# Optimization experiments

Hardware: AMD Instinct MI355X
Metric: run time of the kernel (lower is better)

Reference implementation:

```python
import jax, jax.numpy as jnp
import numpy as np

WINDOW_LEN = 512
N_VAR = 64
LOW_RANK = 16
BATCH = 512


def setup_inputs() -> dict:
    key = jax.random.key(0)
    k_x, k_g, k_b, k_A, k_B = jax.random.split(key, 5)
    x = jax.random.normal(k_x, (BATCH, WINDOW_LEN, N_VAR, 1), dtype=jnp.float32)
    # gating initialized at gating_init in the module; use small positive values
    gating = 0.01 * jnp.ones((N_VAR,), dtype=jnp.float32)
    # bias initialized to zeros in the module, but give it random values so the
    # residual path is exercised numerically
    bias = 0.02 * jax.random.normal(k_b, (WINDOW_LEN, N_VAR), dtype=jnp.float32)
    # kaiming-uniform-ish scale for lora_A: bound = sqrt(6 / fan_in) / sqrt(1+a^2) with a=sqrt(5)
    bound = np.sqrt(6.0 / LOW_RANK) / np.sqrt(6.0)
    lora_A = jax.random.uniform(k_A, (WINDOW_LEN, LOW_RANK), dtype=jnp.float32,
                                minval=-bound, maxval=bound)
    # lora_B is zero-init in the module; use small random values for a nontrivial test
    lora_B = 0.02 * jax.random.normal(k_B, (LOW_RANK, WINDOW_LEN, N_VAR), dtype=jnp.float32)
    return {"x": x, "gating": gating, "bias": bias, "lora_A": lora_A, "lora_B": lora_B}


def reference(x, gating, bias, lora_A, lora_B):
    # x: [b, t, n, d] with t == window_len and n*d == n_var (var_wise=True path)
    b, t, n, d = x.shape
    xr = x.reshape(b, t, n * d)                     # [b, t, v]
    x1 = jnp.tanh(gating * xr)                      # gate per variable, [b, t, v]
    # Original computes weight = einsum('ik,kjl->ijl', lora_A, lora_B)  (dense [t,t,v])
    # then einsum('biv,iov->bov', x1, weight). Same math via associativity:
    tmp = jnp.einsum('biv,ik->bkv', x1, lora_A)     # [b, r, v]
    new_x = jnp.einsum('bkv,kov->bov', tmp, lora_B) # [b, t, v]
    out = xr + new_x + bias                          # residual + bias
    return out.reshape(b, t, n, d)
```

## Files before the change

kernel.cpp:

```cpp
#include <hip/hip_runtime.h>

#define WL 512
#define NV 64
#define LR 16
#define NB 512

__device__ __forceinline__ float tanh_fast(float x) {
    float e = __expf(2.0f * x);
    return 1.0f - 2.0f / (e + 1.0f);
}

__global__ __launch_bounds__(512, 2) void k_tmp(
    const float* __restrict__ x, const float* __restrict__ gating,
    const float* __restrict__ A, float* __restrict__ tmp)
{
    __shared__ float A_lds[WL * LR];
    __shared__ float red[8 * LR * NV];
    const int tid = threadIdx.x;
    const int b = blockIdx.x;

    {
        const float4* src = (const float4*)(A + tid * LR);
        float4* dst = (float4*)(A_lds + tid * LR);
        dst[0] = src[0]; dst[1] = src[1]; dst[2] = src[2]; dst[3] = src[3];
    }
    __syncthreads();

    const int v = tid & 63;
    const int tg = tid >> 6;
    const float g = gating[v];
    float acc[LR];
#pragma unroll
    for (int k = 0; k < LR; ++k) acc[k] = 0.f;

    const float* xb = x + (size_t)b * WL * NV;
    for (int i = 0; i < 64; ++i) {
        const int t = tg * 64 + i;
        const float x1 = tanh_fast(g * xb[t * NV + v]);
        const float* Ar = &A_lds[t * LR];
#pragma unroll
        for (int k = 0; k < LR; ++k) acc[k] += x1 * Ar[k];
    }

#pragma unroll
    for (int k = 0; k < LR; ++k) red[(tg * LR + k) * NV + v] = acc[k];
    __syncthreads();
#pragma unroll
    for (int p = tid; p < LR * NV; p += 512) {
        float s = 0.f;
#pragma unroll
        for (int t = 0; t < 8; ++t) s += red[t * (LR * NV) + p];
        tmp[(size_t)b * (LR * NV) + p] = s;
    }
}

__global__ __launch_bounds__(256, 4) void k_out(
    const float* __restrict__ x, const float* __restrict__ bias,
    const float* __restrict__ Bm, const float* __restrict__ tmp,
    float* __restrict__ out)
{
    const int tid = threadIdx.x;
    const int v = tid & 63;
    const int og = tid >> 6;
    const int o_base = blockIdx.y * 16 + og * 4;
    const int b0 = blockIdx.x * 8;

    float Breg[4][LR];
#pragma unroll
    for (int j = 0; j < 4; ++j) {
        const int o = o_base + j;
#pragma unroll
        for (int k = 0; k < LR; ++k)
            Breg[j][k] = Bm[((size_t)k * WL + o) * NV + v];
    }
    float breg[4];
#pragma unroll
    for (int j = 0; j < 4; ++j) breg[j] = bias[(o_base + j) * NV + v];

    for (int bi = 0; bi < 8; ++bi) {
        const int b = b0 + bi;
        const float* tb = tmp + (size_t)b * (LR * NV) + v;
        float tr[LR];
#pragma unroll
        for (int k = 0; k < LR; ++k) tr[k] = tb[k * NV];
        const float* xb = x + (size_t)b * WL * NV;
        float* ob = out + (size_t)b * WL * NV;
#pragma unroll
        for (int j = 0; j < 4; ++j) {
            const int o = o_base + j;
            float acc = breg[j];
#pragma unroll
            for (int k = 0; k < LR; ++k) acc += tr[k] * Breg[j][k];
            ob[o * NV + v] = xb[o * NV + v] + acc;
        }
    }
}

extern "C" void kernel_launch(void* const* d_in, const int* in_sizes, int n_in,
                              void* d_out, int out_size, void* d_ws, size_t ws_size,
                              hipStream_t stream) {
    const float* x      = (const float*)d_in[0];
    const float* gating = (const float*)d_in[1];
    const float* bias   = (const float*)d_in[2];
    const float* A      = (const float*)d_in[3];
    const float* Bm     = (const float*)d_in[4];
    float* out = (float*)d_out;
    float* tmp = (float*)d_ws;

    k_tmp<<<NB, 512, 0, stream>>>(x, gating, A, tmp);
    k_out<<<dim3(64, 32), 256, 0, stream>>>(x, bias, Bm, tmp, out);
}
```

Baseline: 51.97 us.

## Software-prefetch x and tmp loads, use nontemporal I/O, double batches per block

In k_tmp, x values are loaded in chunks of 8 with the next chunk prefetched into registers, and the occupancy hint is raised to 4 blocks per SM. In k_out, each block handles 16 batches instead of 8, with the next batch's tmp row prefetched, and x reads and out writes use nontemporal builtins. The goal is to hide global memory latency and amortise the register-resident B loads over more batches. The cost is higher register pressure and half as many k_out blocks, which may reduce parallelism.

Measured after the change: 56.18 us. +8.1%, slower.

```diff
diff --git a/kernel.cpp b/kernel.cpp
--- a/kernel.cpp
+++ b/kernel.cpp
@@ -10,7 +10,7 @@
     return 1.0f - 2.0f / (e + 1.0f);
 }
 
-__global__ __launch_bounds__(512, 2) void k_tmp(
+__global__ __launch_bounds__(512, 4) void k_tmp(
     const float* __restrict__ x, const float* __restrict__ gating,
     const float* __restrict__ A, float* __restrict__ tmp)
 {
@@ -33,13 +33,28 @@
 #pragma unroll
     for (int k = 0; k < LR; ++k) acc[k] = 0.f;
 
-    const float* xb = x + (size_t)b * WL * NV;
-    for (int i = 0; i < 64; ++i) {
-        const int t = tg * 64 + i;
-        const float x1 = tanh_fast(g * xb[t * NV + v]);
-        const float* Ar = &A_lds[t * LR];
+    const float* xb = x + (size_t)b * (WL * NV) + (size_t)(tg * 64) * NV + v;
+
+    float cur[8], nxt[8];
 #pragma unroll
-        for (int k = 0; k < LR; ++k) acc[k] += x1 * Ar[k];
+    for (int i = 0; i < 8; ++i) cur[i] = xb[i * NV];
+
+    for (int c = 0; c < 64; c += 8) {
+        if (c + 8 < 64) {
+#pragma unroll
+            for (int i = 0; i < 8; ++i) nxt[i] = xb[(c + 8 + i) * NV];
+        }
+#pragma unroll
+        for (int i = 0; i < 8; ++i) {
+            const float x1 = tanh_fast(g * cur[i]);
+            const float* Ar = &A_lds[(tg * 64 + c + i) * LR];
+#pragma unroll
+            for (int k = 0; k < LR; ++k) acc[k] += x1 * Ar[k];
+        }
+        if (c + 8 < 64) {
+#pragma unroll
+            for (int i = 0; i < 8; ++i) cur[i] = nxt[i];
+        }
     }
 
 #pragma unroll
@@ -63,7 +78,7 @@
     const int v = tid & 63;
     const int og = tid >> 6;
     const int o_base = blockIdx.y * 16 + og * 4;
-    const int b0 = blockIdx.x * 8;
+    const int b0 = blockIdx.x * 16;
 
     float Breg[4][LR];
 #pragma unroll
@@ -77,21 +92,40 @@
 #pragma unroll
     for (int j = 0; j < 4; ++j) breg[j] = bias[(o_base + j) * NV + v];
 
-    for (int bi = 0; bi < 8; ++bi) {
-        const int b = b0 + bi;
-        const float* tb = tmp + (size_t)b * (LR * NV) + v;
-        float tr[LR];
+    float tr[LR], trn[LR];
+    {
+        const float* tb = tmp + (size_t)b0 * (LR * NV) + v;
 #pragma unroll
         for (int k = 0; k < LR; ++k) tr[k] = tb[k * NV];
+    }
+
+    for (int bi = 0; bi < 16; ++bi) {
+        const int b = b0 + bi;
         const float* xb = x + (size_t)b * WL * NV;
         float* ob = out + (size_t)b * WL * NV;
+
+        float xr[4];
+#pragma unroll
+        for (int j = 0; j < 4; ++j)
+            xr[j] = __builtin_nontemporal_load(&xb[(o_base + j) * NV + v]);
+
+        if (bi < 15) {
+            const float* tbn = tmp + (size_t)(b + 1) * (LR * NV) + v;
+#pragma unroll
+            for (int k = 0; k < LR; ++k) trn[k] = tbn[k * NV];
+        }
+
 #pragma unroll
         for (int j = 0; j < 4; ++j) {
-            const int o = o_base + j;
             float acc = breg[j];
 #pragma unroll
             for (int k = 0; k < LR; ++k) acc += tr[k] * Breg[j][k];
-            ob[o * NV + v] = xb[o * NV + v] + acc;
+            __builtin_nontemporal_store(xr[j] + acc, &ob[(o_base + j) * NV + v]);
+        }
+
+        if (bi < 15) {
+#pragma unroll
+            for (int k = 0; k < LR; ++k) tr[k] = trn[k];
         }
     }
 }
@@ -108,5 +142,5 @@
     float* tmp = (float*)d_ws;
 
     k_tmp<<<NB, 512, 0, stream>>>(x, gating, A, tmp);
-    k_out<<<dim3(64, 32), 256, 0, stream>>>(x, bias, Bm, tmp, out);
+    k_out<<<dim3(32, 32), 256, 0, stream>>>(x, bias, Bm, tmp, out);
 }
```
